# Optimization experiments

Measured on AMD Instinct MI355X. Metric: run time of the kernel, lower is better.

The kernel has to match this reference:

```python
import jax, jax.numpy as jnp
import numpy as np

N_NODES = 100000
N_EDGES = 1600000
N_GRAPHS = 512
IN_F, H1, H2 = 128, 128, 256
N_GROUPS, N_FAM = 16, 10


def setup_inputs() -> dict:
    key = jax.random.key(0)
    ks = jax.random.split(key, 8)
    x = jax.random.normal(ks[0], (N_NODES, IN_F), dtype=jnp.float32)
    edge_index = jax.random.randint(ks[1], (2, N_EDGES), 0, N_NODES, dtype=jnp.int64)
    batch = jnp.sort(jax.random.randint(ks[2], (N_NODES,), 0, N_GRAPHS, dtype=jnp.int64))
    W1 = jax.random.normal(ks[3], (IN_F, H1), dtype=jnp.float32) / np.sqrt(IN_F)
    b1 = jnp.zeros((H1,), dtype=jnp.float32)
    W2 = jax.random.normal(ks[4], (H1, H2), dtype=jnp.float32) / np.sqrt(H1)
    b2 = jnp.zeros((H2,), dtype=jnp.float32)
    Wg = jax.random.normal(ks[5], (H2, N_GROUPS), dtype=jnp.float32) / np.sqrt(H2)
    bg = jnp.zeros((N_GROUPS,), dtype=jnp.float32)
    Wf = jax.random.normal(ks[6], (N_GROUPS, H2, N_FAM), dtype=jnp.float32) / np.sqrt(H2)
    bf = jnp.zeros((N_GROUPS, N_FAM), dtype=jnp.float32)
    return {"x": x, "edge_index": edge_index, "batch": batch,
            "W1": W1, "b1": b1, "W2": W2, "b2": b2,
            "Wg": Wg, "bg": bg, "Wf": Wf, "bf": bf}


def gcn_conv(x, W, b, src, dst, num_nodes):
    # PyG GCNConv: add self-loops, symmetric normalization, scatter-add aggregation.
    xw = x @ W  # [N, out]
    deg = jax.ops.segment_sum(jnp.ones((src.shape[0],), x.dtype), dst,
                              num_segments=num_nodes) + 1.0  # +1 self-loop
    dinv = jax.lax.rsqrt(deg)
    coef = dinv[src] * dinv[dst]            # [E]
    msg = xw[src] * coef[:, None]           # gather + scale (memory-bound)
    agg = jax.ops.segment_sum(msg, dst, num_segments=num_nodes)
    agg = agg + xw * (dinv * dinv)[:, None]  # self-loop contribution
    return agg + b


def reference(x, edge_index, batch, W1, b1, W2, b2, Wg, bg, Wf, bf):
    src, dst = edge_index[0], edge_index[1]
    h = jax.nn.relu(gcn_conv(x, W1, b1, src, dst, N_NODES))
    # dropout p=0.5 is identity in eval mode
    h = gcn_conv(h, W2, b2, src, dst, N_NODES)
    # global mean pool over graphs
    sums = jax.ops.segment_sum(h, batch, num_segments=N_GRAPHS)       # [G, H2]
    cnts = jax.ops.segment_sum(jnp.ones((N_NODES,), h.dtype), batch,
                               num_segments=N_GRAPHS)
    pooled = sums / jnp.maximum(cnts, 1.0)[:, None]
    group_logits = pooled @ Wg + bg                                   # [G, num_groups]
    family_logits = jnp.einsum('bd,gdf->gbf', pooled, Wf) + bf[:, None, :]
    return group_logits, family_logits
```

## Files before the change

### kernel.cpp

```cpp
#include <hip/hip_runtime.h>

#define NN 100000
#define NE 1600000
#define NGR 512
#define KF 128
#define H2F 256
#define NGRP 16
#define NFAM 10

#define CH 128
#define NCHUNK ((NN + CH - 1) / CH)
#define PT 6656
#define NT ((NE + PT - 1) / PT)
#define PREPB_BLKS 64

typedef __attribute__((ext_vector_type(8))) short short8;
typedef __attribute__((ext_vector_type(4))) float floatx4;
typedef __attribute__((ext_vector_type(2))) float floatx2;

__device__ __forceinline__ unsigned short f2bf(float f) {
  unsigned u = __float_as_uint(f);
  unsigned r = (u + 0x7fff + ((u >> 16) & 1)) >> 16;
  return (unsigned short)r;
}
__device__ __forceinline__ float2 bf2f(unsigned u) {
  float2 r;
  r.x = __uint_as_float(u << 16);
  r.y = __uint_as_float(u & 0xffff0000u);
  return r;
}
__device__ __forceinline__ unsigned short pk_fp8(float a, float b) {
  return (unsigned short)__builtin_amdgcn_cvt_pk_fp8_f32(a, b, 0, false);
}
__device__ __forceinline__ floatx2 unpk_fp8(unsigned short u) {
  return __builtin_amdgcn_cvt_pk_f32_fp8((int)u, false);
}


__global__ __launch_bounds__(256) void k_histprep(const int* __restrict__ ei,
                                                  int* __restrict__ tot,
                                                  const float* __restrict__ W,
                                                  unsigned short* __restrict__ Bp) {
  __shared__ int lh[NCHUNK];
  int tid = threadIdx.x;
  if (blockIdx.x >= NT) {
    int idx = (blockIdx.x - NT) * 256 + tid;
    int j = idx & 7;
    int l = (idx >> 3) & 63;
    int rest = idx >> 9;
    int nc = rest & 7;
    int kc = rest >> 3;
    int k = kc * 32 + (l >> 4) * 8 + j;
    int nn = nc * 16 + (l & 15);
    Bp[idx] = f2bf(W[k * KF + nn]);
    return;
  }
  for (int g = tid; g < NCHUNK; g += 256) lh[g] = 0;
  __syncthreads();
  int base = blockIdx.x * PT;
  int nv = min(PT, NE - base);
  for (int i = tid; i < nv; i += 256) atomicAdd(&lh[ei[NE + base + i] >> 7], 1);
  __syncthreads();
  for (int g = tid; g < NCHUNK; g += 256) {
    int v = lh[g];
    if (v) atomicAdd(&tot[g], v);
  }
}


__global__ __launch_bounds__(256) void k_scantot(const int* __restrict__ tot,
                                                 int* __restrict__ cbase,
                                                 int* __restrict__ cursor) {
  __shared__ int ssc[256];
  int tid = threadIdx.x;
  int v4[4]; int loc = 0;
#pragma unroll
  for (int j = 0; j < 4; ++j) {
    int idx = tid * 4 + j;
    v4[j] = (idx < NCHUNK) ? tot[idx] : 0;
    loc += v4[j];
  }
  ssc[tid] = loc;
  __syncthreads();
  for (int off = 1; off < 256; off <<= 1) {
    int val = (tid >= off) ? ssc[tid - off] : 0;
    __syncthreads();
    ssc[tid] += val;
    __syncthreads();
  }
  int excl = ssc[tid] - loc;
#pragma unroll
  for (int j = 0; j < 4; ++j) {
    int idx = tid * 4 + j;
    if (idx < NCHUNK) { cbase[idx] = excl; cursor[idx] = excl; }
    excl += v4[j];
  }
  if (tid == 255) cbase[NCHUNK] = excl;
}


__global__ __launch_bounds__(256) void k_pscatter(const int* __restrict__ ei,
                                                  int* __restrict__ cursor,
                                                  int2* __restrict__ erec) {
  __shared__ int2 stage[PT];
  __shared__ int lstart[NCHUNK];
  __shared__ int lrun[NCHUNK];
  __shared__ int gbase[NCHUNK];
  __shared__ int ssc[256];
  int t0 = blockIdx.x, tid = threadIdx.x;
  for (int g = tid; g < NCHUNK; g += 256) lrun[g] = 0;
  __syncthreads();
  int base = t0 * PT;
  int nv = min(PT, NE - base);
  for (int i = tid; i < nv; i += 256) atomicAdd(&lrun[ei[NE + base + i] >> 7], 1);
  __syncthreads();
  int v4[4]; int loc = 0;
#pragma unroll
  for (int j = 0; j < 4; ++j) {
    int idx = tid * 4 + j;
    v4[j] = (idx < NCHUNK) ? lrun[idx] : 0;
    loc += v4[j];
  }
  ssc[tid] = loc;
  __syncthreads();
  for (int off = 1; off < 256; off <<= 1) {
    int val = (tid >= off) ? ssc[tid - off] : 0;
    __syncthreads();
    ssc[tid] += val;
    __syncthreads();
  }
  int excl = ssc[tid] - loc;
#pragma unroll
  for (int j = 0; j < 4; ++j) {
    int idx = tid * 4 + j;
    if (idx < NCHUNK) lstart[idx] = excl;
    excl += v4[j];
  }
  __syncthreads();
  for (int g = tid; g < NCHUNK; g += 256) {
    int cnt = ((g + 1 < NCHUNK) ? lstart[g + 1] : nv) - lstart[g];
    gbase[g] = cnt ? atomicAdd(&cursor[g], cnt) : 0;
    lrun[g] = lstart[g];
  }
  __syncthreads();
  for (int i = tid; i < nv; i += 256) {
    int s = ei[base + i], d = ei[NE + base + i];
    int pos = atomicAdd(&lrun[d >> 7], 1);
    stage[pos] = make_int2(s, d);
  }
  __syncthreads();
  for (int j = tid; j < nv; j += 256) {
    int2 r = stage[j];
    int g = r.y >> 7;
    erec[gbase[g] + (j - lstart[g])] = r;
  }
}


__global__ __launch_bounds__(256) void k_sort(const int2* __restrict__ erec,
                                              const int* __restrict__ cbase,
                                              int* __restrict__ esrc,
                                              int* __restrict__ rowptr,
                                              float* __restrict__ dinv) {
  __shared__ int hist[CH];
  __shared__ int lrun[CH];
  __shared__ int sc[256];
  const int c = blockIdx.x, tid = threadIdx.x;
  const int e0 = cbase[c], e1 = cbase[c + 1];
  const int nv = e1 - e0;
  if (tid < CH) hist[tid] = 0;
  __syncthreads();
  for (int i = tid; i < nv; i += 256) atomicAdd(&hist[erec[e0 + i].y & (CH - 1)], 1);
  __syncthreads();
  int deg = (tid < CH) ? hist[tid] : 0;
  sc[tid] = deg;
  __syncthreads();
  for (int off = 1; off < 256; off <<= 1) {
    int val = (tid >= off) ? sc[tid - off] : 0;
    __syncthreads();
    sc[tid] += val;
    __syncthreads();
  }
  int excl = sc[tid] - deg;
  int node = c * CH + tid;
  if (tid < CH) {
    lrun[tid] = excl;
    if (node < NN) {
      rowptr[node] = e0 + excl;
      dinv[node] = rsqrtf((float)(deg + 1));
    } else if (node == NN) {
      rowptr[NN] = e0 + excl;
    }
  }
  __syncthreads();
  for (int i = tid; i < nv; i += 256) {
    int2 r = erec[e0 + i];
    int pos = atomicAdd(&lrun[r.y & (CH - 1)], 1);
    esrc[e0 + pos] = r.x;
  }
}


__global__ __launch_bounds__(256) void k_gemm_mfma(const float* __restrict__ A,
                                                   const unsigned short* __restrict__ Bp,
                                                   const float* __restrict__ dinv,
                                                   unsigned short* __restrict__ C) {
  constexpr int K = 128;
  constexpr int NCH = KF / 16;
  const int wv = blockIdx.x * 4 + (threadIdx.x >> 6);
  const int row0 = wv * 16;
  if (row0 >= NN) return;
  const int lane = threadIdx.x & 63;
  const int m = lane & 15;
  const int q = lane >> 4;

  floatx4 acc[NCH];
#pragma unroll
  for (int i = 0; i < NCH; ++i) acc[i] = (floatx4){0.f, 0.f, 0.f, 0.f};

  const int arow = row0 + m;
#pragma unroll
  for (int kc = 0; kc < 4; ++kc) {
    const float* ap = A + (size_t)arow * K + kc * 32 + q * 8;
    float4 f0 = *(const float4*)ap;
    float4 f1 = *(const float4*)(ap + 4);
    short8 af;
    af[0] = (short)f2bf(f0.x); af[1] = (short)f2bf(f0.y);
    af[2] = (short)f2bf(f0.z); af[3] = (short)f2bf(f0.w);
    af[4] = (short)f2bf(f1.x); af[5] = (short)f2bf(f1.y);
    af[6] = (short)f2bf(f1.z); af[7] = (short)f2bf(f1.w);
    const unsigned short* bp = Bp + (size_t)kc * NCH * 512;
#pragma unroll
    for (int nc = 0; nc < NCH; ++nc) {
      short8 bfr = *(const short8*)(bp + (size_t)nc * 512 + lane * 8);
      acc[nc] = __builtin_amdgcn_mfma_f32_16x16x32_bf16(af, bfr, acc[nc], 0, 0, 0);
    }
  }

  float ds[4];
#pragma unroll
  for (int r = 0; r < 4; ++r) ds[r] = dinv[row0 + q * 4 + r];
#pragma unroll
  for (int nc = 0; nc < 4; ++nc) {
#pragma unroll
    for (int r = 0; r < 4; ++r) {
      int row = row0 + q * 4 + r;
      C[(size_t)row * 64 + nc * 16 + m] =
          pk_fp8(acc[nc][r] * ds[r], acc[nc + 4][r] * ds[r]);
    }
  }
}


template <bool FIRST>
__global__ __launch_bounds__(128) void k_agg(const unsigned short* __restrict__ p,
                                             const float* __restrict__ bias,
                                             const int* __restrict__ rowptr,
                                             const int* __restrict__ esrc,
                                             const float* __restrict__ dinv,
                                             void* __restrict__ outp) {
  const int n = blockIdx.x * 2 + (threadIdx.x >> 6);
  const int t = threadIdx.x & 63;
  const int u = t & 31;
  const int half = t >> 5;
  const unsigned* __restrict__ prow = (const unsigned*)p;

  float a0 = 0.f, a1 = 0.f, a2 = 0.f, a3 = 0.f;

  if (half == 0) {
    unsigned v = prow[((unsigned)n << 5) + u];
    floatx2 lo = unpk_fp8((unsigned short)(v & 0xffffu));
    floatx2 hi = unpk_fp8((unsigned short)(v >> 16));
    a0 = lo.x; a1 = lo.y; a2 = hi.x; a3 = hi.y;
  }

  const int r0 = rowptr[n];
  const int r1 = rowptr[n + 1];
  int i = r0;

#define PAIR_TIER(NP)                                                  \
  for (; i + 2 * (NP) <= r1; i += 2 * (NP)) {                          \
    const int ib = i + half;                                           \
    unsigned s[NP];                                                    \
    _Pragma("unroll") for (int j = 0; j < (NP); ++j)                   \
        s[j] = (unsigned)esrc[ib + 2 * j];                             \
    unsigned v[NP];                                                    \
    _Pragma("unroll") for (int j = 0; j < (NP); ++j)                   \
        v[j] = prow[(s[j] << 5) + u];                                  \
    _Pragma("unroll") for (int j = 0; j < (NP); ++j) {                 \
      floatx2 lo = unpk_fp8((unsigned short)(v[j] & 0xffffu));         \
      floatx2 hi = unpk_fp8((unsigned short)(v[j] >> 16));             \
      a0 += lo.x; a1 += lo.y; a2 += hi.x; a3 += hi.y;                  \
    }                                                                  \
  }

  PAIR_TIER(8)
  PAIR_TIER(4)
  PAIR_TIER(2)
  PAIR_TIER(1)
#undef PAIR_TIER

  if (i < r1 && half == 0) {
    unsigned s = (unsigned)esrc[i];
    unsigned v = prow[(s << 5) + u];
    floatx2 lo = unpk_fp8((unsigned short)(v & 0xffffu));
    floatx2 hi = unpk_fp8((unsigned short)(v >> 16));
    a0 += lo.x; a1 += lo.y; a2 += hi.x; a3 += hi.y;
  }

  a0 += __shfl_down(a0, 32, 64);
  a1 += __shfl_down(a1, 32, 64);
  a2 += __shfl_down(a2, 32, 64);
  a3 += __shfl_down(a3, 32, 64);

  if (half == 0) {
    const float dn = dinv[n];
    if (FIRST) {
      float2 blo = *(const float2*)(bias + 2 * u);
      float2 bhi = *(const float2*)(bias + 64 + 2 * u);
      float x0 = fmaxf(fmaf(dn, a0, blo.x), 0.f) * dn;
      float x1 = fmaxf(fmaf(dn, a1, bhi.x), 0.f) * dn;
      float x2 = fmaxf(fmaf(dn, a2, blo.y), 0.f) * dn;
      float x3 = fmaxf(fmaf(dn, a3, bhi.y), 0.f) * dn;
      unsigned lo = pk_fp8(x0, x1);
      unsigned hi = pk_fp8(x2, x3);
      ((unsigned*)outp)[((unsigned)n << 5) + u] = lo | (hi << 16);
    } else {
      float x0 = a0 * dn, x1 = a1 * dn, x2 = a2 * dn, x3 = a3 * dn;
      uint2 w;
      w.x = (unsigned)f2bf(x0) | ((unsigned)f2bf(x1) << 16);
      w.y = (unsigned)f2bf(x2) | ((unsigned)f2bf(x3) << 16);
      ((uint2*)outp)[((unsigned)n << 5) + u] = w;
    }
  }
}


__global__ __launch_bounds__(256) void k_poolheads(const unsigned* __restrict__ hp,
                                                   const int* __restrict__ batch,
                                                   const float* __restrict__ W2,
                                                   const float* __restrict__ b2,
                                                   const float* __restrict__ Wg,
                                                   const float* __restrict__ bg,
                                                   const float* __restrict__ Wf,
                                                   const float* __restrict__ bfb,
                                                   float* __restrict__ out) {
  __shared__ float sh[4][128];
  __shared__ float pr[KF];
  __shared__ float p[H2F];
  __shared__ int bnd[2];
  const int g = blockIdx.x;
  const int tid = threadIdx.x;
  if (tid < 2) {
    int target = g + tid;
    int lo = 0, hi = NN;
    while (lo < hi) { int mid = (lo + hi) >> 1; if (batch[mid] < target) lo = mid + 1; else hi = mid; }
    bnd[tid] = lo;
  }
  __syncthreads();
  const int start = bnd[0], end = bnd[1];
  const int t = tid & 63, wv = tid >> 6;

  float sx = 0.f, sy = 0.f;
  int n = start + wv;
  for (; n + 12 < end; n += 16) {
    unsigned u0 = hp[(size_t)n * 64 + t];
    unsigned u1 = hp[(size_t)(n + 4) * 64 + t];
    unsigned u2 = hp[(size_t)(n + 8) * 64 + t];
    unsigned u3 = hp[(size_t)(n + 12) * 64 + t];
    float2 f0 = bf2f(u0), f1 = bf2f(u1), f2 = bf2f(u2), f3 = bf2f(u3);
    sx += (f0.x + f1.x) + (f2.x + f3.x);
    sy += (f0.y + f1.y) + (f2.y + f3.y);
  }
  for (; n < end; n += 4) {
    float2 f = bf2f(hp[(size_t)n * 64 + t]);
    sx += f.x; sy += f.y;
  }
  sh[wv][2 * t] = sx;
  sh[wv][2 * t + 1] = sy;
  __syncthreads();
  if (wv == 0) {
    float vx = sh[0][2 * t] + sh[1][2 * t] + sh[2][2 * t] + sh[3][2 * t];
    float vy = sh[0][2 * t + 1] + sh[1][2 * t + 1] + sh[2][2 * t + 1] + sh[3][2 * t + 1];
    float c = fmaxf((float)(end - start), 1.f);
    pr[t] = vx / c;
    pr[t + 64] = vy / c;
  }
  __syncthreads();
  float acc = b2[tid];
#pragma unroll 8
  for (int d = 0; d < KF; ++d) acc = fmaf(pr[d], W2[d * H2F + tid], acc);
  p[tid] = acc;
  __syncthreads();
  if (tid < NGRP) {
    float a = bg[tid];
    for (int d = 0; d < H2F; ++d) a = fmaf(p[d], Wg[d * NGRP + tid], a);
    out[g * NGRP + tid] = a;
  } else if (tid >= 64 && tid < 64 + NGRP * NFAM) {
    int u = tid - 64;
    int gg = u / NFAM;
    int ff = u % NFAM;
    float a = bfb[gg * NFAM + ff];
    for (int d = 0; d < H2F; ++d) a = fmaf(p[d], Wf[(gg * H2F + d) * NFAM + ff], a);
    out[NGR * NGRP + (size_t)gg * NGR * NFAM + g * NFAM + ff] = a;
  }
}


extern "C" void kernel_launch(void* const* d_in, const int* in_sizes, int n_in,
                              void* d_out, int out_size, void* d_ws, size_t ws_size,
                              hipStream_t stream) {
  const float* x    = (const float*)d_in[0];
  const int*   ei   = (const int*)d_in[1];
  const int*   batch= (const int*)d_in[2];
  const float* W1   = (const float*)d_in[3];
  const float* b1   = (const float*)d_in[4];
  const float* W2   = (const float*)d_in[5];
  const float* b2   = (const float*)d_in[6];
  const float* Wg   = (const float*)d_in[7];
  const float* bg   = (const float*)d_in[8];
  const float* Wf   = (const float*)d_in[9];
  const float* bfb  = (const float*)d_in[10];
  float* out = (float*)d_out;

  char* w = (char*)d_ws;
  auto take = [&](size_t bytes) {
    char* p = w;
    w += (bytes + 255) & ~(size_t)255;
    return (void*)p;
  };
  int*   tot   = (int*)take((size_t)NCHUNK * 4);
  int*   cbase = (int*)take((size_t)(NCHUNK + 1) * 4);
  int*   cursor= (int*)take((size_t)NCHUNK * 4);
  int2*  erec  = (int2*)take((size_t)NE * 8);
  int*   esrc  = (int*)take((size_t)NE * 4);
  int*   rowptr= (int*)take((size_t)(NN + 1) * 4);
  float* dinv  = (float*)take((size_t)NN * 4);
  unsigned short* Bp1 = (unsigned short*)take((size_t)KF * KF * 2);
  unsigned short* xw1 = (unsigned short*)take((size_t)NN * 64 * 2);
  unsigned short* h1  = (unsigned short*)take((size_t)NN * 64 * 2);
  unsigned* agg2= (unsigned*)take((size_t)NN * KF * 2);

  hipMemsetAsync(tot, 0, (size_t)NCHUNK * 4, stream);
  k_histprep<<<NT + PREPB_BLKS, 256, 0, stream>>>(ei, tot, W1, Bp1);
  k_scantot<<<1, 256, 0, stream>>>(tot, cbase, cursor);
  k_pscatter<<<NT, 256, 0, stream>>>(ei, cursor, erec);
  k_sort<<<NCHUNK, 256, 0, stream>>>(erec, cbase, esrc, rowptr, dinv);

  k_gemm_mfma<<<1563, 256, 0, stream>>>(x, Bp1, dinv, xw1);

  k_agg<true><<<NN / 2, 128, 0, stream>>>(xw1, b1, rowptr, esrc, dinv, h1);
  k_agg<false><<<NN / 2, 128, 0, stream>>>(h1, nullptr, rowptr, esrc, dinv, agg2);

  k_poolheads<<<NGR, 256, 0, stream>>>(agg2, batch, W2, b2, Wg, bg, Wf, bfb, out);
}
```

Measured before the change: 299.5 us.

## Slice feature columns into four planes for cache-resident gather aggregation

The fp8 node features are reorganized into four column slices of 32 bytes per node, written by the GEMM epilogue in that sliced layout. Aggregation blocks now process one slice at a time, so each gather pass touches a 3.2MB working set that can stay resident in L2/LLC. Each wave handles 4 nodes, with 8 edges processed in parallel by 8 lanes apiece, and uses nontemporal loads and stores for the edge stream and outputs. The cost is that the edge indices and rowptr are read four times, and each gather is now 32 bytes instead of 128, which wastes part of every cache line unless the hardware sectors fetches.

```diff
diff --git a/kernel.cpp b/kernel.cpp
--- a/kernel.cpp
+++ b/kernel.cpp
@@ -14,9 +14,13 @@
 #define NT ((NE + PT - 1) / PT)
 #define PREPB_BLKS 64
 
+#define NSLICE 4
+#define BPS (NN / 8)
+
 typedef __attribute__((ext_vector_type(8))) short short8;
 typedef __attribute__((ext_vector_type(4))) float floatx4;
 typedef __attribute__((ext_vector_type(2))) float floatx2;
+typedef __attribute__((ext_vector_type(2))) unsigned uintx2;
 
 __device__ __forceinline__ unsigned short f2bf(float f) {
   unsigned u = __float_as_uint(f);
@@ -245,7 +249,7 @@
 #pragma unroll
     for (int r = 0; r < 4; ++r) {
       int row = row0 + q * 4 + r;
-      C[(size_t)row * 64 + nc * 16 + m] =
+      C[((size_t)nc * NN + row) * 16 + m] =
           pk_fp8(acc[nc][r] * ds[r], acc[nc + 4][r] * ds[r]);
     }
   }
@@ -253,84 +257,89 @@
 
 
 template <bool FIRST>
-__global__ __launch_bounds__(128) void k_agg(const unsigned short* __restrict__ p,
+__global__ __launch_bounds__(128) void k_agg(const unsigned* __restrict__ ps,
                                              const float* __restrict__ bias,
                                              const int* __restrict__ rowptr,
                                              const int* __restrict__ esrc,
                                              const float* __restrict__ dinv,
                                              void* __restrict__ outp) {
-  const int n = blockIdx.x * 2 + (threadIdx.x >> 6);
-  const int t = threadIdx.x & 63;
-  const int u = t & 31;
-  const int half = t >> 5;
-  const unsigned* __restrict__ prow = (const unsigned*)p;
-
-  float a0 = 0.f, a1 = 0.f, a2 = 0.f, a3 = 0.f;
-
-  if (half == 0) {
-    unsigned v = prow[((unsigned)n << 5) + u];
-    floatx2 lo = unpk_fp8((unsigned short)(v & 0xffffu));
-    floatx2 hi = unpk_fp8((unsigned short)(v >> 16));
-    a0 = lo.x; a1 = lo.y; a2 = hi.x; a3 = hi.y;
-  }
-
-  const int r0 = rowptr[n];
-  const int r1 = rowptr[n + 1];
-  int i = r0;
-
-#define PAIR_TIER(NP)                                                  \
-  for (; i + 2 * (NP) <= r1; i += 2 * (NP)) {                          \
-    const int ib = i + half;                                           \
-    unsigned s[NP];                                                    \
-    _Pragma("unroll") for (int j = 0; j < (NP); ++j)                   \
-        s[j] = (unsigned)esrc[ib + 2 * j];                             \
-    unsigned v[NP];                                                    \
-    _Pragma("unroll") for (int j = 0; j < (NP); ++j)                   \
-        v[j] = prow[(s[j] << 5) + u];                                  \
-    _Pragma("unroll") for (int j = 0; j < (NP); ++j) {                 \
-      floatx2 lo = unpk_fp8((unsigned short)(v[j] & 0xffffu));         \
-      floatx2 hi = unpk_fp8((unsigned short)(v[j] >> 16));             \
-      a0 += lo.x; a1 += lo.y; a2 += hi.x; a3 += hi.y;                  \
-    }                                                                  \
-  }
-
-  PAIR_TIER(8)
-  PAIR_TIER(4)
-  PAIR_TIER(2)
-  PAIR_TIER(1)
-#undef PAIR_TIER
-
-  if (i < r1 && half == 0) {
-    unsigned s = (unsigned)esrc[i];
-    unsigned v = prow[(s << 5) + u];
-    floatx2 lo = unpk_fp8((unsigned short)(v & 0xffffu));
-    floatx2 hi = unpk_fp8((unsigned short)(v >> 16));
-    a0 += lo.x; a1 += lo.y; a2 += hi.x; a3 += hi.y;
-  }
-
-  a0 += __shfl_down(a0, 32, 64);
-  a1 += __shfl_down(a1, 32, 64);
-  a2 += __shfl_down(a2, 32, 64);
-  a3 += __shfl_down(a3, 32, 64);
-
-  if (half == 0) {
-    const float dn = dinv[n];
-    if (FIRST) {
-      float2 blo = *(const float2*)(bias + 2 * u);
-      float2 bhi = *(const float2*)(bias + 64 + 2 * u);
-      float x0 = fmaxf(fmaf(dn, a0, blo.x), 0.f) * dn;
-      float x1 = fmaxf(fmaf(dn, a1, bhi.x), 0.f) * dn;
-      float x2 = fmaxf(fmaf(dn, a2, blo.y), 0.f) * dn;
-      float x3 = fmaxf(fmaf(dn, a3, bhi.y), 0.f) * dn;
-      unsigned lo = pk_fp8(x0, x1);
-      unsigned hi = pk_fp8(x2, x3);
-      ((unsigned*)outp)[((unsigned)n << 5) + u] = lo | (hi << 16);
+  const int s  = blockIdx.x / BPS;
+  const int bs = blockIdx.x % BPS;
+  const int t  = threadIdx.x & 63;
+  const int e  = t >> 3;
+  const int d  = t & 7;
+  const unsigned* __restrict__ pslice = ps + (size_t)s * NN * 8;
+  const int n0 = (bs * 2 + (threadIdx.x >> 6)) * 4;
+
+  for (int nl = 0; nl < 4; ++nl) {
+    const int n = n0 + nl;
+    float a0, a1, a2, a3;
+    if (t < 8) {
+      unsigned v = pslice[((unsigned)n << 3) + d];
+      floatx2 lo = unpk_fp8((unsigned short)(v & 0xffffu));
+      floatx2 hi = unpk_fp8((unsigned short)(v >> 16));
+      a0 = lo.x; a1 = lo.y; a2 = hi.x; a3 = hi.y;
     } else {
-      float x0 = a0 * dn, x1 = a1 * dn, x2 = a2 * dn, x3 = a3 * dn;
-      uint2 w;
-      w.x = (unsigned)f2bf(x0) | ((unsigned)f2bf(x1) << 16);
-      w.y = (unsigned)f2bf(x2) | ((unsigned)f2bf(x3) << 16);
-      ((uint2*)outp)[((unsigned)n << 5) + u] = w;
+      a0 = 0.f; a1 = 0.f; a2 = 0.f; a3 = 0.f;
+    }
+
+    const int r0 = rowptr[n];
+    const int r1 = rowptr[n + 1];
+    int i = r0;
+    for (; i + 16 <= r1; i += 16) {
+      int s0 = __builtin_nontemporal_load(esrc + i + e);
+      int s1 = __builtin_nontemporal_load(esrc + i + 8 + e);
+      unsigned v0 = pslice[((unsigned)s0 << 3) + d];
+      unsigned v1 = pslice[((unsigned)s1 << 3) + d];
+      floatx2 f;
+      f = unpk_fp8((unsigned short)(v0 & 0xffffu)); a0 += f.x; a1 += f.y;
+      f = unpk_fp8((unsigned short)(v0 >> 16));     a2 += f.x; a3 += f.y;
+      f = unpk_fp8((unsigned short)(v1 & 0xffffu)); a0 += f.x; a1 += f.y;
+      f = unpk_fp8((unsigned short)(v1 >> 16));     a2 += f.x; a3 += f.y;
+    }
+    for (; i + 8 <= r1; i += 8) {
+      int s0 = __builtin_nontemporal_load(esrc + i + e);
+      unsigned v0 = pslice[((unsigned)s0 << 3) + d];
+      floatx2 f;
+      f = unpk_fp8((unsigned short)(v0 & 0xffffu)); a0 += f.x; a1 += f.y;
+      f = unpk_fp8((unsigned short)(v0 >> 16));     a2 += f.x; a3 += f.y;
+    }
+    int rem = r1 - i;
+    if (e < rem) {
+      int s0 = __builtin_nontemporal_load(esrc + i + e);
+      unsigned v0 = pslice[((unsigned)s0 << 3) + d];
+      floatx2 f;
+      f = unpk_fp8((unsigned short)(v0 & 0xffffu)); a0 += f.x; a1 += f.y;
+      f = unpk_fp8((unsigned short)(v0 >> 16));     a2 += f.x; a3 += f.y;
+    }
+
+    a0 += __shfl_xor(a0, 8, 64);  a1 += __shfl_xor(a1, 8, 64);
+    a2 += __shfl_xor(a2, 8, 64);  a3 += __shfl_xor(a3, 8, 64);
+    a0 += __shfl_xor(a0, 16, 64); a1 += __shfl_xor(a1, 16, 64);
+    a2 += __shfl_xor(a2, 16, 64); a3 += __shfl_xor(a3, 16, 64);
+    a0 += __shfl_xor(a0, 32, 64); a1 += __shfl_xor(a1, 32, 64);
+    a2 += __shfl_xor(a2, 32, 64); a3 += __shfl_xor(a3, 32, 64);
+
+    if (t < 8) {
+      const float dn = dinv[n];
+      if (FIRST) {
+        const int tb = s * 16 + 2 * d;
+        float x0 = fmaxf(fmaf(dn, a0, bias[tb]), 0.f) * dn;
+        float x1 = fmaxf(fmaf(dn, a1, bias[tb + 64]), 0.f) * dn;
+        float x2 = fmaxf(fmaf(dn, a2, bias[tb + 1]), 0.f) * dn;
+        float x3 = fmaxf(fmaf(dn, a3, bias[tb + 65]), 0.f) * dn;
+        unsigned lo = pk_fp8(x0, x1);
+        unsigned hi = pk_fp8(x2, x3);
+        __builtin_nontemporal_store(lo | (hi << 16),
+            (unsigned*)outp + (size_t)s * NN * 8 + ((unsigned)n << 3) + d);
+      } else {
+        float x0 = a0 * dn, x1 = a1 * dn, x2 = a2 * dn, x3 = a3 * dn;
+        uintx2 w;
+        w.x = (unsigned)f2bf(x0) | ((unsigned)f2bf(x1) << 16);
+        w.y = (unsigned)f2bf(x2) | ((unsigned)f2bf(x3) << 16);
+        __builtin_nontemporal_store(w,
+            (uintx2*)outp + (size_t)n * 32 + s * 8 + d);
+      }
     }
   }
 }
@@ -449,8 +458,8 @@
 
   k_gemm_mfma<<<1563, 256, 0, stream>>>(x, Bp1, dinv, xw1);
 
-  k_agg<true><<<NN / 2, 128, 0, stream>>>(xw1, b1, rowptr, esrc, dinv, h1);
-  k_agg<false><<<NN / 2, 128, 0, stream>>>(h1, nullptr, rowptr, esrc, dinv, agg2);
+  k_agg<true><<<NSLICE * BPS, 128, 0, stream>>>((const unsigned*)xw1, b1, rowptr, esrc, dinv, h1);
+  k_agg<false><<<NSLICE * BPS, 128, 0, stream>>>((const unsigned*)h1, nullptr, rowptr, esrc, dinv, agg2);
 
   k_poolheads<<<NGR, 256, 0, stream>>>(agg2, batch, W2, b2, Wg, bg, Wf, bfb, out);
 }
```

After: 518.3 us. 1.73x slower.

## Make GCN aggregation persistent grid-stride with prefetched row metadata and nontemporal accesses

Applied to the files above, without the earlier changes.

Turns the two aggregation kernels into persistent grid-stride loops: 2048 blocks of 256 threads, four nodes per block at a time, striding across all nodes instead of launching one block per node pair. The next node's rowptr bounds and dinv are prefetched while the current node is processed. Edge-index loads and output stores now use nontemporal hints so they avoid polluting cache needed for the gathered feature rows. This cuts block-launch overhead and hides metadata latency, but a fixed grid can leave load imbalance with skewed degrees and may lower occupancy.

```diff
diff --git a/kernel.cpp b/kernel.cpp
--- a/kernel.cpp
+++ b/kernel.cpp
@@ -14,9 +14,12 @@
 #define NT ((NE + PT - 1) / PT)
 #define PREPB_BLKS 64
 
+#define AGG_BLKS 2048
+
 typedef __attribute__((ext_vector_type(8))) short short8;
 typedef __attribute__((ext_vector_type(4))) float floatx4;
 typedef __attribute__((ext_vector_type(2))) float floatx2;
+typedef __attribute__((ext_vector_type(2))) unsigned uintx2;
 
 __device__ __forceinline__ unsigned short f2bf(float f) {
   unsigned u = __float_as_uint(f);
@@ -253,85 +256,103 @@
 
 
 template <bool FIRST>
-__global__ __launch_bounds__(128) void k_agg(const unsigned short* __restrict__ p,
+__global__ __launch_bounds__(256) void k_agg(const unsigned short* __restrict__ p,
                                              const float* __restrict__ bias,
                                              const int* __restrict__ rowptr,
                                              const int* __restrict__ esrc,
                                              const float* __restrict__ dinv,
                                              void* __restrict__ outp) {
-  const int n = blockIdx.x * 2 + (threadIdx.x >> 6);
+  const int nw = AGG_BLKS * 4;
+  int n = blockIdx.x * 4 + (threadIdx.x >> 6);
   const int t = threadIdx.x & 63;
   const int u = t & 31;
   const int half = t >> 5;
   const unsigned* __restrict__ prow = (const unsigned*)p;
-
-  float a0 = 0.f, a1 = 0.f, a2 = 0.f, a3 = 0.f;
-
-  if (half == 0) {
-    unsigned v = prow[((unsigned)n << 5) + u];
-    floatx2 lo = unpk_fp8((unsigned short)(v & 0xffffu));
-    floatx2 hi = unpk_fp8((unsigned short)(v >> 16));
-    a0 = lo.x; a1 = lo.y; a2 = hi.x; a3 = hi.y;
-  }
-
-  const int r0 = rowptr[n];
-  const int r1 = rowptr[n + 1];
-  int i = r0;
+  if (n >= NN) return;
+
+  int r0 = rowptr[n];
+  int r1 = rowptr[n + 1];
+  float dn = dinv[n];
+
+  while (1) {
+    const int nn = n + nw;
+    const bool more = (nn < NN);
+    int r0n = 0, r1n = 0;
+    float dnn = 0.f;
+    if (more) {
+      r0n = rowptr[nn];
+      r1n = rowptr[nn + 1];
+      dnn = dinv[nn];
+    }
+
+    float a0 = 0.f, a1 = 0.f, a2 = 0.f, a3 = 0.f;
+    if (half == 0) {
+      unsigned v = prow[((unsigned)n << 5) + u];
+      floatx2 lo = unpk_fp8((unsigned short)(v & 0xffffu));
+      floatx2 hi = unpk_fp8((unsigned short)(v >> 16));
+      a0 = lo.x; a1 = lo.y; a2 = hi.x; a3 = hi.y;
+    }
+
+    int i = r0;
 
 #define PAIR_TIER(NP)                                                  \
-  for (; i + 2 * (NP) <= r1; i += 2 * (NP)) {                          \
-    const int ib = i + half;                                           \
-    unsigned s[NP];                                                    \
-    _Pragma("unroll") for (int j = 0; j < (NP); ++j)                   \
-        s[j] = (unsigned)esrc[ib + 2 * j];                             \
-    unsigned v[NP];                                                    \
-    _Pragma("unroll") for (int j = 0; j < (NP); ++j)                   \
-        v[j] = prow[(s[j] << 5) + u];                                  \
-    _Pragma("unroll") for (int j = 0; j < (NP); ++j) {                 \
-      floatx2 lo = unpk_fp8((unsigned short)(v[j] & 0xffffu));         \
-      floatx2 hi = unpk_fp8((unsigned short)(v[j] >> 16));             \
-      a0 += lo.x; a1 += lo.y; a2 += hi.x; a3 += hi.y;                  \
-    }                                                                  \
-  }
-
-  PAIR_TIER(8)
-  PAIR_TIER(4)
-  PAIR_TIER(2)
-  PAIR_TIER(1)
+    for (; i + 2 * (NP) <= r1; i += 2 * (NP)) {                        \
+      const int ib = i + half;                                         \
+      unsigned s[NP];                                                  \
+      _Pragma("unroll") for (int j = 0; j < (NP); ++j)                 \
+          s[j] = (unsigned)__builtin_nontemporal_load(esrc + ib + 2 * j); \
+      unsigned v[NP];                                                  \
+      _Pragma("unroll") for (int j = 0; j < (NP); ++j)                 \
+          v[j] = prow[(s[j] << 5) + u];                                \
+      _Pragma("unroll") for (int j = 0; j < (NP); ++j) {               \
+        floatx2 lo = unpk_fp8((unsigned short)(v[j] & 0xffffu));       \
+        floatx2 hi = unpk_fp8((unsigned short)(v[j] >> 16));           \
+        a0 += lo.x; a1 += lo.y; a2 += hi.x; a3 += hi.y;                \
+      }                                                                \
+    }
+
+    PAIR_TIER(8)
+    PAIR_TIER(4)
+    PAIR_TIER(2)
+    PAIR_TIER(1)
 #undef PAIR_TIER
 
-  if (i < r1 && half == 0) {
-    unsigned s = (unsigned)esrc[i];
-    unsigned v = prow[(s << 5) + u];
-    floatx2 lo = unpk_fp8((unsigned short)(v & 0xffffu));
-    floatx2 hi = unpk_fp8((unsigned short)(v >> 16));
-    a0 += lo.x; a1 += lo.y; a2 += hi.x; a3 += hi.y;
-  }
-
-  a0 += __shfl_down(a0, 32, 64);
-  a1 += __shfl_down(a1, 32, 64);
-  a2 += __shfl_down(a2, 32, 64);
-  a3 += __shfl_down(a3, 32, 64);
-
-  if (half == 0) {
-    const float dn = dinv[n];
-    if (FIRST) {
-      float2 blo = *(const float2*)(bias + 2 * u);
-      float2 bhi = *(const float2*)(bias + 64 + 2 * u);
-      float x0 = fmaxf(fmaf(dn, a0, blo.x), 0.f) * dn;
-      float x1 = fmaxf(fmaf(dn, a1, bhi.x), 0.f) * dn;
-      float x2 = fmaxf(fmaf(dn, a2, blo.y), 0.f) * dn;
-      float x3 = fmaxf(fmaf(dn, a3, bhi.y), 0.f) * dn;
-      unsigned lo = pk_fp8(x0, x1);
-      unsigned hi = pk_fp8(x2, x3);
-      ((unsigned*)outp)[((unsigned)n << 5) + u] = lo | (hi << 16);
-    } else {
-      float x0 = a0 * dn, x1 = a1 * dn, x2 = a2 * dn, x3 = a3 * dn;
-      uint2 w;
-      w.x = (unsigned)f2bf(x0) | ((unsigned)f2bf(x1) << 16);
-      w.y = (unsigned)f2bf(x2) | ((unsigned)f2bf(x3) << 16);
-      ((uint2*)outp)[((unsigned)n << 5) + u] = w;
-    }
+    if (i < r1 && half == 0) {
+      unsigned s = (unsigned)__builtin_nontemporal_load(esrc + i);
+      unsigned v = prow[(s << 5) + u];
+      floatx2 lo = unpk_fp8((unsigned short)(v & 0xffffu));
+      floatx2 hi = unpk_fp8((unsigned short)(v >> 16));
+      a0 += lo.x; a1 += lo.y; a2 += hi.x; a3 += hi.y;
+    }
+
+    a0 += __shfl_down(a0, 32, 64);
+    a1 += __shfl_down(a1, 32, 64);
+    a2 += __shfl_down(a2, 32, 64);
+    a3 += __shfl_down(a3, 32, 64);
+
+    if (half == 0) {
+      if (FIRST) {
+        float2 blo = *(const float2*)(bias + 2 * u);
+        float2 bhi = *(const float2*)(bias + 64 + 2 * u);
+        float x0 = fmaxf(fmaf(dn, a0, blo.x), 0.f) * dn;
+        float x1 = fmaxf(fmaf(dn, a1, bhi.x), 0.f) * dn;
+        float x2 = fmaxf(fmaf(dn, a2, blo.y), 0.f) * dn;
+        float x3 = fmaxf(fmaf(dn, a3, bhi.y), 0.f) * dn;
+        unsigned lo = pk_fp8(x0, x1);
+        unsigned hi = pk_fp8(x2, x3);
+        __builtin_nontemporal_store(lo | (hi << 16),
+            (unsigned*)outp + ((unsigned)n << 5) + u);
+      } else {
+        float x0 = a0 * dn, x1 = a1 * dn, x2 = a2 * dn, x3 = a3 * dn;
+        uintx2 w;
+        w.x = (unsigned)f2bf(x0) | ((unsigned)f2bf(x1) << 16);
+        w.y = (unsigned)f2bf(x2) | ((unsigned)f2bf(x3) << 16);
+        __builtin_nontemporal_store(w, (uintx2*)outp + ((unsigned)n << 5) + u);
+      }
+    }
+
+    if (!more) break;
+    n = nn; r0 = r0n; r1 = r1n; dn = dnn;
   }
 }
 
@@ -449,8 +470,8 @@
 
   k_gemm_mfma<<<1563, 256, 0, stream>>>(x, Bp1, dinv, xw1);
 
-  k_agg<true><<<NN / 2, 128, 0, stream>>>(xw1, b1, rowptr, esrc, dinv, h1);
-  k_agg<false><<<NN / 2, 128, 0, stream>>>(h1, nullptr, rowptr, esrc, dinv, agg2);
+  k_agg<true><<<AGG_BLKS, 256, 0, stream>>>(xw1, b1, rowptr, esrc, dinv, h1);
+  k_agg<false><<<AGG_BLKS, 256, 0, stream>>>(h1, nullptr, rowptr, esrc, dinv, agg2);
 
   k_poolheads<<<NGR, 256, 0, stream>>>(agg2, batch, W2, b2, Wg, bg, Wf, bfb, out);
 }
```

After: 320.2 us. 1.07x slower.

## Build CSR with global per-node degree atomics and a direct edge scatter

Applied to the files above, without the earlier changes.

Replaces the two-pass bucketed counting sort (a chunk-level partition scatter through an intermediate edge-record buffer, then a per-chunk local sort) with per-node degree counting via global atomics in the histogram kernel. A per-chunk scan then sets rowptr, cursors and dinv, and a simple kernel scatters each source index into place using an atomic on a per-node cursor. This removes the 12.8MB intermediate buffer and one pass over the edges. In exchange it adds 1.6M global atomics in the histogram pass and 1.6M more in the scatter, with random write positions, and the order of edges within each row becomes nondeterministic.

```diff
diff --git a/kernel.cpp b/kernel.cpp
--- a/kernel.cpp
+++ b/kernel.cpp
@@ -17,6 +17,7 @@
 typedef __attribute__((ext_vector_type(8))) short short8;
 typedef __attribute__((ext_vector_type(4))) float floatx4;
 typedef __attribute__((ext_vector_type(2))) float floatx2;
+typedef __attribute__((ext_vector_type(2))) unsigned uintx2;
 
 __device__ __forceinline__ unsigned short f2bf(float f) {
   unsigned u = __float_as_uint(f);
@@ -39,6 +40,7 @@
 
 __global__ __launch_bounds__(256) void k_histprep(const int* __restrict__ ei,
                                                   int* __restrict__ tot,
+                                                  int* __restrict__ nodedeg,
                                                   const float* __restrict__ W,
                                                   unsigned short* __restrict__ Bp) {
   __shared__ int lh[NCHUNK];
@@ -59,7 +61,11 @@
   __syncthreads();
   int base = blockIdx.x * PT;
   int nv = min(PT, NE - base);
-  for (int i = tid; i < nv; i += 256) atomicAdd(&lh[ei[NE + base + i] >> 7], 1);
+  for (int i = tid; i < nv; i += 256) {
+    int d = ei[NE + base + i];
+    atomicAdd(&lh[d >> 7], 1);
+    atomicAdd(&nodedeg[d], 1);
+  }
   __syncthreads();
   for (int g = tid; g < NCHUNK; g += 256) {
     int v = lh[g];
@@ -69,8 +75,7 @@
 
 
 __global__ __launch_bounds__(256) void k_scantot(const int* __restrict__ tot,
-                                                 int* __restrict__ cbase,
-                                                 int* __restrict__ cursor) {
+                                                 int* __restrict__ cbase) {
   __shared__ int ssc[256];
   int tid = threadIdx.x;
   int v4[4]; int loc = 0;
@@ -92,112 +97,49 @@
 #pragma unroll
   for (int j = 0; j < 4; ++j) {
     int idx = tid * 4 + j;
-    if (idx < NCHUNK) { cbase[idx] = excl; cursor[idx] = excl; }
+    if (idx < NCHUNK) cbase[idx] = excl;
     excl += v4[j];
   }
   if (tid == 255) cbase[NCHUNK] = excl;
 }
 
 
-__global__ __launch_bounds__(256) void k_pscatter(const int* __restrict__ ei,
-                                                  int* __restrict__ cursor,
-                                                  int2* __restrict__ erec) {
-  __shared__ int2 stage[PT];
-  __shared__ int lstart[NCHUNK];
-  __shared__ int lrun[NCHUNK];
-  __shared__ int gbase[NCHUNK];
-  __shared__ int ssc[256];
-  int t0 = blockIdx.x, tid = threadIdx.x;
-  for (int g = tid; g < NCHUNK; g += 256) lrun[g] = 0;
-  __syncthreads();
-  int base = t0 * PT;
-  int nv = min(PT, NE - base);
-  for (int i = tid; i < nv; i += 256) atomicAdd(&lrun[ei[NE + base + i] >> 7], 1);
-  __syncthreads();
-  int v4[4]; int loc = 0;
-#pragma unroll
-  for (int j = 0; j < 4; ++j) {
-    int idx = tid * 4 + j;
-    v4[j] = (idx < NCHUNK) ? lrun[idx] : 0;
-    loc += v4[j];
-  }
-  ssc[tid] = loc;
-  __syncthreads();
-  for (int off = 1; off < 256; off <<= 1) {
-    int val = (tid >= off) ? ssc[tid - off] : 0;
-    __syncthreads();
-    ssc[tid] += val;
-    __syncthreads();
-  }
-  int excl = ssc[tid] - loc;
-#pragma unroll
-  for (int j = 0; j < 4; ++j) {
-    int idx = tid * 4 + j;
-    if (idx < NCHUNK) lstart[idx] = excl;
-    excl += v4[j];
-  }
-  __syncthreads();
-  for (int g = tid; g < NCHUNK; g += 256) {
-    int cnt = ((g + 1 < NCHUNK) ? lstart[g + 1] : nv) - lstart[g];
-    gbase[g] = cnt ? atomicAdd(&cursor[g], cnt) : 0;
-    lrun[g] = lstart[g];
-  }
-  __syncthreads();
-  for (int i = tid; i < nv; i += 256) {
-    int s = ei[base + i], d = ei[NE + base + i];
-    int pos = atomicAdd(&lrun[d >> 7], 1);
-    stage[pos] = make_int2(s, d);
-  }
-  __syncthreads();
-  for (int j = tid; j < nv; j += 256) {
-    int2 r = stage[j];
-    int g = r.y >> 7;
-    erec[gbase[g] + (j - lstart[g])] = r;
-  }
-}
-
-
-__global__ __launch_bounds__(256) void k_sort(const int2* __restrict__ erec,
-                                              const int* __restrict__ cbase,
-                                              int* __restrict__ esrc,
-                                              int* __restrict__ rowptr,
-                                              float* __restrict__ dinv) {
-  __shared__ int hist[CH];
-  __shared__ int lrun[CH];
-  __shared__ int sc[256];
+__global__ __launch_bounds__(CH) void k_nodescan(const int* __restrict__ nodedeg,
+                                                 const int* __restrict__ cbase,
+                                                 int* __restrict__ rowptr,
+                                                 int* __restrict__ cursor,
+                                                 float* __restrict__ dinv) {
+  __shared__ int sc[CH];
   const int c = blockIdx.x, tid = threadIdx.x;
-  const int e0 = cbase[c], e1 = cbase[c + 1];
-  const int nv = e1 - e0;
-  if (tid < CH) hist[tid] = 0;
-  __syncthreads();
-  for (int i = tid; i < nv; i += 256) atomicAdd(&hist[erec[e0 + i].y & (CH - 1)], 1);
-  __syncthreads();
-  int deg = (tid < CH) ? hist[tid] : 0;
+  const int node = c * CH + tid;
+  const int deg = (node < NN) ? nodedeg[node] : 0;
   sc[tid] = deg;
   __syncthreads();
-  for (int off = 1; off < 256; off <<= 1) {
+  for (int off = 1; off < CH; off <<= 1) {
     int val = (tid >= off) ? sc[tid - off] : 0;
     __syncthreads();
     sc[tid] += val;
     __syncthreads();
   }
-  int excl = sc[tid] - deg;
-  int node = c * CH + tid;
-  if (tid < CH) {
-    lrun[tid] = excl;
-    if (node < NN) {
-      rowptr[node] = e0 + excl;
-      dinv[node] = rsqrtf((float)(deg + 1));
-    } else if (node == NN) {
-      rowptr[NN] = e0 + excl;
-    }
-  }
-  __syncthreads();
-  for (int i = tid; i < nv; i += 256) {
-    int2 r = erec[e0 + i];
-    int pos = atomicAdd(&lrun[r.y & (CH - 1)], 1);
-    esrc[e0 + pos] = r.x;
-  }
+  const int excl = sc[tid] - deg + cbase[c];
+  if (node < NN) {
+    rowptr[node] = excl;
+    cursor[node] = excl;
+    dinv[node] = rsqrtf((float)(deg + 1));
+  }
+  if (c == NCHUNK - 1 && tid == 0) rowptr[NN] = NE;
+}
+
+
+__global__ __launch_bounds__(256) void k_escatter(const int* __restrict__ ei,
+                                                  int* __restrict__ cursor,
+                                                  int* __restrict__ esrc) {
+  const int i = blockIdx.x * 256 + threadIdx.x;
+  if (i >= NE) return;
+  const int s = ei[i];
+  const int d = ei[NE + i];
+  const int pos = atomicAdd(&cursor[d], 1);
+  esrc[pos] = s;
 }
 
 
@@ -327,10 +269,10 @@
       ((unsigned*)outp)[((unsigned)n << 5) + u] = lo | (hi << 16);
     } else {
       float x0 = a0 * dn, x1 = a1 * dn, x2 = a2 * dn, x3 = a3 * dn;
-      uint2 w;
+      uintx2 w;
       w.x = (unsigned)f2bf(x0) | ((unsigned)f2bf(x1) << 16);
       w.y = (unsigned)f2bf(x2) | ((unsigned)f2bf(x3) << 16);
-      ((uint2*)outp)[((unsigned)n << 5) + u] = w;
+      ((uintx2*)outp)[((unsigned)n << 5) + u] = w;
     }
   }
 }
@@ -429,23 +371,25 @@
     w += (bytes + 255) & ~(size_t)255;
     return (void*)p;
   };
-  int*   tot   = (int*)take((size_t)NCHUNK * 4);
-  int*   cbase = (int*)take((size_t)(NCHUNK + 1) * 4);
-  int*   cursor= (int*)take((size_t)NCHUNK * 4);
-  int2*  erec  = (int2*)take((size_t)NE * 8);
-  int*   esrc  = (int*)take((size_t)NE * 4);
-  int*   rowptr= (int*)take((size_t)(NN + 1) * 4);
-  float* dinv  = (float*)take((size_t)NN * 4);
+  int*   tot    = (int*)take((size_t)NCHUNK * 4);
+  int*   nodedeg= (int*)take((size_t)NN * 4);
+  int*   cbase  = (int*)take((size_t)(NCHUNK + 1) * 4);
+  int*   cursor = (int*)take((size_t)NN * 4);
+  int*   esrc   = (int*)take((size_t)NE * 4);
+  int*   rowptr = (int*)take((size_t)(NN + 1) * 4);
+  float* dinv   = (float*)take((size_t)NN * 4);
   unsigned short* Bp1 = (unsigned short*)take((size_t)KF * KF * 2);
   unsigned short* xw1 = (unsigned short*)take((size_t)NN * 64 * 2);
   unsigned short* h1  = (unsigned short*)take((size_t)NN * 64 * 2);
   unsigned* agg2= (unsigned*)take((size_t)NN * KF * 2);
 
-  hipMemsetAsync(tot, 0, (size_t)NCHUNK * 4, stream);
-  k_histprep<<<NT + PREPB_BLKS, 256, 0, stream>>>(ei, tot, W1, Bp1);
-  k_scantot<<<1, 256, 0, stream>>>(tot, cbase, cursor);
-  k_pscatter<<<NT, 256, 0, stream>>>(ei, cursor, erec);
-  k_sort<<<NCHUNK, 256, 0, stream>>>(erec, cbase, esrc, rowptr, dinv);
+  size_t zbytes = (size_t)((char*)nodedeg - (char*)tot) + (size_t)NN * 4;
+  hipMemsetAsync(tot, 0, zbytes, stream);
+
+  k_histprep<<<NT + PREPB_BLKS, 256, 0, stream>>>(ei, tot, nodedeg, W1, Bp1);
+  k_scantot<<<1, 256, 0, stream>>>(tot, cbase);
+  k_nodescan<<<NCHUNK, CH, 0, stream>>>(nodedeg, cbase, rowptr, cursor, dinv);
+  k_escatter<<<(NE + 255) / 256, 256, 0, stream>>>(ei, cursor, esrc);
 
   k_gemm_mfma<<<1563, 256, 0, stream>>>(x, Bp1, dinv, xw1);
 
```

After: 439.8 us. +46.9%, slower.
